# Optimization experiments

Hardware: AMD Instinct MI355X
Metric: run time of the kernel (lower is better)

The kernel has to match this reference:

```python
import jax, jax.numpy as jnp
import numpy as np

B, T_ENC, T_DEC, E = 16, 512, 128, 512
H = 1024


def setup_inputs() -> dict:
    key = jax.random.key(0)
    ks = jax.random.split(key, 16)
    def rn(k, shape, s=0.02):
        return jax.random.normal(k, shape, jnp.float32) * s
    z = lambda *s: jnp.zeros(s, jnp.float32)
    return {
        "inputs": jax.random.normal(ks[0], (B, T_ENC, E), jnp.float32),
        "padded_mels": jax.random.normal(ks[1], (B, 80, T_DEC), jnp.float32),
        "W_enc": rn(ks[2], (128, E)),
        "W_q": rn(ks[3], (128, H)),
        "W_loc_conv": rn(ks[4], (32, 1, 31)),
        "b_loc_conv": z(32),
        "W_loc_dense": rn(ks[5], (128, 32)),
        "b_loc_dense": z(128),
        "w_e": rn(ks[6], (1, 128)),
        "b_e": z(1),
        "W_p1": rn(ks[7], (256, 80)),
        "W_p2": rn(ks[8], (256, 256)),
        "W_ih1": rn(ks[9], (4 * H, 256 + E)),
        "W_hh1": rn(ks[10], (4 * H, H)),
        "b_ih1": z(4 * H),
        "b_hh1": z(4 * H),
        "W_ih2": rn(ks[11], (4 * H, H)),
        "W_hh2": rn(ks[12], (4 * H, H)),
        "b_ih2": z(4 * H),
        "b_hh2": z(4 * H),
        "W_proj": rn(ks[13], (80, H + E)),
        "b_proj": z(80),
        "W_stop": rn(ks[14], (1, H + E)),
        "b_stop": z(1),
    }


def _lstm_cell(x, h, c, W_ih, W_hh, b_ih, b_hh):
    g = W_ih @ x + b_ih + W_hh @ h + b_hh
    i, f, gg, o = jnp.split(g, 4)  # torch gate order: i, f, g, o
    c = jax.nn.sigmoid(f) * c + jax.nn.sigmoid(i) * jnp.tanh(gg)
    h = jax.nn.sigmoid(o) * jnp.tanh(c)
    return h, c


def _forward(inputs, padded_mels, W_enc, W_q, W_loc_conv, b_loc_conv,
             W_loc_dense, b_loc_dense, w_e, b_e, W_p1, W_p2,
             W_ih1, W_hh1, b_ih1, b_hh1, W_ih2, W_hh2, b_ih2, b_hh2,
             W_proj, b_proj, W_stop, b_stop):
    proc_enc = inputs @ W_enc.T  # (B, T_enc, 128)
    # prepend zero frame, use frames 0..T_dec-1 as teacher-forced inputs
    prev = jnp.concatenate([jnp.zeros((B, 80, 1), inputs.dtype), padded_mels], axis=-1)[:, :, :T_DEC]
    prev = jnp.transpose(prev, (2, 0, 1))  # (T_dec, B, 80)
    # F.dropout(p=0.5) in source defaults to training=True -> always applied; deterministic masks here
    mk = jax.random.key(42)
    m1 = jax.random.bernoulli(jax.random.fold_in(mk, 0), 0.5, (T_DEC, B, 256)).astype(inputs.dtype) * 2.0
    m2 = jax.random.bernoulli(jax.random.fold_in(mk, 1), 0.5, (T_DEC, B, 256)).astype(inputs.dtype) * 2.0

    def lstm2(x_seq):
        # faithful to source: (B,1,768) fed to batch_first=False nn.LSTM ->
        # sequence runs over the batch dim with batch=1 and zero init state each step
        zv = jnp.zeros((H,), x_seq.dtype)
        def cell(carry, x):
            h1, c1, h2, c2 = carry
            h1, c1 = _lstm_cell(x, h1, c1, W_ih1, W_hh1, b_ih1, b_hh1)
            h2, c2 = _lstm_cell(h1, h2, c2, W_ih2, W_hh2, b_ih2, b_hh2)
            return (h1, c1, h2, c2), h2
        _, hs = jax.lax.scan(cell, (zv, zv, zv, zv), x_seq)
        return hs  # (B, 1024)

    def step(carry, xs):
        cum, ctx = carry  # (B, T_enc), (B, E)
        x, d1, d2 = xs
        p = jax.nn.relu(x @ W_p1.T) * d1
        p = jax.nn.relu(p @ W_p2.T) * d2
        h = lstm2(jnp.concatenate([p, ctx], axis=-1))  # (B, 1024)
        q = h @ W_q.T  # (B, 128)
        loc = jax.lax.conv_general_dilated(
            cum[:, None, :], W_loc_conv, (1,), [(15, 15)],
            dimension_numbers=("NCH", "OIH", "NCH")) + b_loc_conv[None, :, None]  # (B, 32, T_enc)
        loc = jnp.transpose(loc, (0, 2, 1)) @ W_loc_dense.T + b_loc_dense  # (B, T_enc, 128)
        e = jnp.tanh(q[:, None, :] + loc + proc_enc) @ w_e[0] + b_e[0]  # (B, T_enc)
        aw = jax.nn.softmax(e, axis=1)
        new_ctx = jnp.einsum("bt,bte->be", aw, inputs)  # (B, E)
        do = jnp.concatenate([h, new_ctx], axis=-1)  # (B, 1536)
        frame = do @ W_proj.T + b_proj  # (B, 80)
        stop = do @ W_stop[0] + b_stop[0]  # (B,)
        return (cum + aw, new_ctx), (frame, stop)

    carry0 = (jnp.zeros((B, T_ENC), inputs.dtype), jnp.zeros((B, E), inputs.dtype))
    _, (mels, stops) = jax.lax.scan(step, carry0, (prev, m1, m2))
    return jnp.transpose(mels, (1, 0, 2)), jnp.transpose(stops, (1, 0))


def reference(inputs, padded_mels, W_enc, W_q, W_loc_conv, b_loc_conv,
              W_loc_dense, b_loc_dense, w_e, b_e, W_p1, W_p2,
              W_ih1, W_hh1, b_ih1, b_hh1, W_ih2, W_hh2, b_ih2, b_hh2,
              W_proj, b_proj, W_stop, b_stop):
    return _forward(inputs, padded_mels, W_enc, W_q, W_loc_conv, b_loc_conv,
                    W_loc_dense, b_loc_dense, w_e, b_e, W_p1, W_p2,
                    W_ih1, W_hh1, b_ih1, b_hh1, W_ih2, W_hh2, b_ih2, b_hh2,
                    W_proj, b_proj, W_stop, b_stop)
```

## Files before the change

kernel.cpp:

```cpp
#include <hip/hip_runtime.h>
#include <hip/hip_bf16.h>
#include <stdint.h>

#define TD 128
#define NB 16
#define TE 512
#define EE 512
#define HH 1024
#define NM 80
#define PP 256
#define NWG 256
#define NTH 512

#define AGENT __HIP_MEMORY_SCOPE_AGENT

__device__ inline float aloadf(const float* p) {
  return __hip_atomic_load(p, __ATOMIC_RELAXED, AGENT);
}
__device__ inline void astoref(float* p, float v) {
  __hip_atomic_store(p, v, __ATOMIC_RELAXED, AGENT);
}
__device__ inline double aloadd(const double* p) {
  return __hip_atomic_load(p, __ATOMIC_RELAXED, AGENT);
}
__device__ inline void astored(double* p, double v) {
  __hip_atomic_store(p, v, __ATOMIC_RELAXED, AGENT);
}
__device__ inline float2 aload2f(const float* p) {
  unsigned long long v =
      __hip_atomic_load((const unsigned long long*)p, __ATOMIC_RELAXED, AGENT);
  union { unsigned long long u; float2 f; } c; c.u = v; return c.f;
}
__device__ inline double dsig(double x) { return 1.0 / (1.0 + exp(-x)); }

__host__ __device__ inline void threefry2x32(uint32_t k0, uint32_t k1,
                                             uint32_t& x0, uint32_t& x1) {
  uint32_t ks0 = k0, ks1 = k1, ks2 = k0 ^ k1 ^ 0x1BD11BDAu;
  x0 += ks0; x1 += ks1;
#define RND(rot) { x0 += x1; x1 = (x1 << (rot)) | (x1 >> (32 - (rot))); x1 ^= x0; }
  RND(13) RND(15) RND(26) RND(6)
  x0 += ks1; x1 += ks2 + 1u;
  RND(17) RND(29) RND(16) RND(24)
  x0 += ks2; x1 += ks0 + 2u;
  RND(13) RND(15) RND(26) RND(6)
  x0 += ks0; x1 += ks1 + 3u;
  RND(17) RND(29) RND(16) RND(24)
  x0 += ks1; x1 += ks2 + 4u;
  RND(13) RND(15) RND(26) RND(6)
  x0 += ks2; x1 += ks0 + 5u;
#undef RND
}

__device__ inline double mask_val(uint32_t ka, uint32_t kb, uint32_t i) {
  uint32_t x0 = 0u, x1 = i;
  threefry2x32(ka, kb, x0, x1);
  uint32_t bits = x0 ^ x1;
  float u = __uint_as_float((bits >> 9) | 0x3f800000u) - 1.0f;
  return (u < 0.5f) ? 2.0 : 0.0;
}

__global__ void k_proc_enc(const float* __restrict__ inputs,
                           const float* __restrict__ W_enc,
                           float* __restrict__ procTf) {
  int blk = blockIdx.x;
  int b = blk >> 5;
  int t0 = (blk & 31) * 16;
  int d = threadIdx.x;
  __shared__ float in_l[16][EE];
  for (int idx = threadIdx.x; idx < 16 * EE; idx += blockDim.x) {
    int tt = idx >> 9, e = idx & 511;
    in_l[tt][e] = inputs[((size_t)(b * TE + t0 + tt)) * EE + e];
  }
  __syncthreads();
  double acc[16];
#pragma unroll
  for (int tt = 0; tt < 16; ++tt) acc[tt] = 0.0;
  const float* wr = W_enc + (size_t)d * EE;
  for (int e = 0; e < EE; ++e) {
    double w = (double)wr[e];
#pragma unroll
    for (int tt = 0; tt < 16; ++tt) acc[tt] += w * (double)in_l[tt][e];
  }
  for (int tt = 0; tt < 16; ++tt)
    procTf[((size_t)(b * 128 + d)) * TE + t0 + tt] = (float)acc[tt];
}

__global__ void k_p(const float* __restrict__ pm, const float* __restrict__ Wp1,
                    const float* __restrict__ Wp2,
                    uint32_t k1a, uint32_t k1b, uint32_t k2a, uint32_t k2b,
                    float* __restrict__ p_allf) {
  int sb = blockIdx.x;
  int s = sb >> 4, b = sb & 15;
  int tid = threadIdx.x;
  uint32_t mi = (uint32_t)(sb * PP + tid);
  double d1 = mask_val(k1a, k1b, mi);
  double d2 = mask_val(k2a, k2b, mi);
  __shared__ float x_l[NM];
  __shared__ double p1_l[PP];
  if (tid < NM) x_l[tid] = (s == 0) ? 0.f : pm[(b * NM + tid) * TD + (s - 1)];
  __syncthreads();
  double a = 0.0;
  const float* w1 = Wp1 + tid * NM;
  for (int m = 0; m < NM; ++m) a += (double)w1[m] * (double)x_l[m];
  a = fmax(a, 0.0) * d1;
  p1_l[tid] = a;
  __syncthreads();
  double c = 0.0;
  const float* w2 = Wp2 + tid * PP;
  for (int k = 0; k < PP; ++k) c += (double)w2[k] * p1_l[k];
  c = fmax(c, 0.0) * d2;
  p_allf[sb * PP + tid] = (float)c;
}

__global__ void k_init(double* __restrict__ cumg, float* __restrict__ ctxf,
                       float* __restrict__ h1f, float* __restrict__ h2f,
                       uint32_t* __restrict__ barmem) {
  int tid = threadIdx.x;
  for (int i = tid; i < NB * TE; i += 256) cumg[i] = 0.0;
  for (int i = tid; i < NB * EE; i += 256) ctxf[i] = 0.f;
  for (int i = tid; i < 2 * HH; i += 256) { h1f[i] = 0.f; h2f[i] = 0.f; }
  for (int i = tid; i < 1024; i += 256) barmem[i] = 0u;
}

struct SMEM {
  float wldT[4096];
  float wcl[992];
  double bld[128], we[128], blc[32];
  double b1l[16], b2l[16];
  double g1l[16][16];
  double gA[16], gBC[16];
  double c1l[4], c2l[4];
  double be0;
  union U {
    struct { float h1[1024], h2[1024]; } cell;
    struct { float h[1024]; } pq;
    struct { float ctxall[8192]; double x[768]; } g1p;
    struct { double cum[64], q[128], loc[32][33]; } att;
    struct { float aw[512]; double red[16][32]; } ctxp;
    struct { double red[16]; } soft;
    struct { float hb[1536]; double red[16]; } outp;
  } u;
};

__device__ inline void gridbar(uint32_t* barmem, uint32_t& lgen, int wg, int tid) {
  __syncthreads();
  lgen++;
  if (tid == 0) {
    int g = wg & 7;
    uint32_t a = __hip_atomic_fetch_add(&barmem[g * 32], 1u, __ATOMIC_RELAXED, AGENT);
    if (a == 31u) {
      uint32_t b = __hip_atomic_fetch_add(&barmem[256], 1u, __ATOMIC_RELAXED, AGENT);
      if (b == 7u) {
        for (int i = 0; i < 8; ++i)
          __hip_atomic_store(&barmem[i * 32], 0u, __ATOMIC_RELAXED, AGENT);
        __hip_atomic_store(&barmem[256], 0u, __ATOMIC_RELAXED, AGENT);
        asm volatile("s_waitcnt vmcnt(0)" ::: "memory");
        __hip_atomic_store(&barmem[288], lgen, __ATOMIC_RELAXED, AGENT);
      }
    }
    while (__hip_atomic_load(&barmem[288], __ATOMIC_RELAXED, AGENT) < lgen)
      __builtin_amdgcn_s_sleep(2);
  }
  __syncthreads();
}

__global__ __launch_bounds__(NTH)
__attribute__((amdgpu_waves_per_eu(2, 2)))
void k_persist(
    const float* __restrict__ inputs,
    const float* __restrict__ W_q,
    const float* __restrict__ W_lc, const float* __restrict__ b_lc,
    const float* __restrict__ W_ld, const float* __restrict__ b_ld,
    const float* __restrict__ w_e, const float* __restrict__ b_e,
    const float* __restrict__ W_ih1, const float* __restrict__ W_hh1,
    const float* __restrict__ b_ih1, const float* __restrict__ b_hh1,
    const float* __restrict__ W_ih2, const float* __restrict__ W_hh2,
    const float* __restrict__ b_ih2, const float* __restrict__ b_hh2,
    const float* __restrict__ W_proj, const float* __restrict__ b_proj,
    const float* __restrict__ W_stop, const float* __restrict__ b_stop,
    const float* __restrict__ p_allf, const float* __restrict__ procTf,
    float* h1f, float* h2f, float* h_allf, float* qf,
    float* ef, float* awf, double* cumg, float* ctxf,
    uint32_t* barmem, float* out) {
  __shared__ SMEM sm;
  const int wg = blockIdx.x, tid = threadIdx.x;
  const int q = tid >> 5, l = tid & 31;
  const int row = (q >> 2) * 1024 + wg * 4 + (q & 3);
  uint32_t lgen = 0;

  for (int i = tid; i < 4096; i += NTH) sm.wldT[(i & 31) * 128 + (i >> 5)] = W_ld[i];
  for (int i = tid; i < 992; i += NTH) sm.wcl[i] = W_lc[i];
  for (int i = tid; i < 128; i += NTH) { sm.bld[i] = (double)b_ld[i]; sm.we[i] = (double)w_e[i]; }
  if (tid < 32) sm.blc[tid] = (double)b_lc[tid];
  if (tid == 0) sm.be0 = (double)b_e[0];
  if (l == 0) {
    sm.b1l[q] = (double)b_ih1[row] + (double)b_hh1[row];
    sm.b2l[q] = (double)b_ih2[row] + (double)b_hh2[row];
  }

  float wA[32], wB[32], wC[32], wD[24];
#pragma unroll
  for (int k = 0; k < 32; ++k) {
    int c = l + 32 * k;
    wA[k] = W_hh1[(size_t)row * 1024 + c];
    wB[k] = W_ih2[(size_t)row * 1024 + c];
    wC[k] = W_hh2[(size_t)row * 1024 + c];
  }
#pragma unroll
  for (int k = 0; k < 24; ++k) wD[k] = W_ih1[(size_t)row * 768 + l + 32 * k];
#pragma unroll
  for (int k = 0; k < 32; ++k) {
    asm volatile("" : "+v"(wA[k]));
    asm volatile("" : "+v"(wB[k]));
    asm volatile("" : "+v"(wC[k]));
  }
#pragma unroll
  for (int k = 0; k < 24; ++k) asm volatile("" : "+v"(wD[k]));
  __syncthreads();

  {
    for (int i = tid; i < 8192; i += NTH) sm.u.g1p.ctxall[i] = aloadf(ctxf + i);
    __syncthreads();
    for (int b = 0; b < 16; ++b) {
      for (int i = tid; i < 768; i += NTH)
        sm.u.g1p.x[i] = (i < 256) ? (double)p_allf[((size_t)0 * 16 + b) * 256 + i]
                                  : (double)sm.u.g1p.ctxall[b * 512 + (i - 256)];
      __syncthreads();
      double a = 0.0;
#pragma unroll
      for (int k = 0; k < 24; ++k) a += (double)wD[k] * sm.u.g1p.x[l + 32 * k];
#pragma unroll
      for (int m = 1; m <= 16; m <<= 1) a += __shfl_xor(a, m);
      if (l == 0) sm.g1l[b][q] = a + sm.b1l[q];
      __syncthreads();
    }
  }
  gridbar(barmem, lgen, wg, tid);

  for (int s = 0; s < TD; ++s) {
    for (int r = 0; r <= 16; ++r) {
      if (r == 0 && tid < 4) { sm.c1l[tid] = 0.0; sm.c2l[tid] = 0.0; }
      {
        float2 v1 = aload2f(h1f + (((r & 1) ^ 1)) * 1024 + 2 * tid);
        sm.u.cell.h1[2 * tid] = v1.x; sm.u.cell.h1[2 * tid + 1] = v1.y;
        if (r > 0) {
          float2 v2 = aload2f(h2f + (r & 1) * 1024 + 2 * tid);
          sm.u.cell.h2[2 * tid] = v2.x; sm.u.cell.h2[2 * tid + 1] = v2.y;
        }
      }
      __syncthreads();

      double a0 = 0.0, a1 = 0.0, a2 = 0.0;
#pragma unroll
      for (int k = 0; k < 32; ++k) {
        double h1v = (double)sm.u.cell.h1[l + 32 * k];
        a0 += (double)wA[k] * h1v;
        a1 += (double)wB[k] * h1v;
        a2 += (double)wC[k] * (double)sm.u.cell.h2[l + 32 * k];
      }
#pragma unroll
      for (int m = 1; m <= 16; m <<= 1) {
        a0 += __shfl_xor(a0, m);
        a1 += __shfl_xor(a1, m);
        a2 += __shfl_xor(a2, m);
      }
      if (l == 0) { sm.gA[q] = a0; sm.gBC[q] = a1 + a2; }
      __syncthreads();

      if (r < 16 && tid < 4) {
        int jj = tid;
        double gi = sm.g1l[r][jj]      + sm.gA[jj];
        double gf = sm.g1l[r][4 + jj]  + sm.gA[4 + jj];
        double gg = sm.g1l[r][8 + jj]  + sm.gA[8 + jj];
        double go = sm.g1l[r][12 + jj] + sm.gA[12 + jj];
        double cn = dsig(gf) * sm.c1l[jj] + dsig(gi) * tanh(gg);
        double hn = dsig(go) * tanh(cn);
        sm.c1l[jj] = cn;
        astoref(h1f + (r & 1) * 1024 + wg * 4 + jj, (float)hn);
      }
      if (r > 0 && tid >= 8 && tid < 12) {
        int jj = tid - 8, b = r - 1;
        double gi = sm.gBC[jj]      + sm.b2l[jj];
        double gf = sm.gBC[4 + jj]  + sm.b2l[4 + jj];
        double gg = sm.gBC[8 + jj]  + sm.b2l[8 + jj];
        double go = sm.gBC[12 + jj] + sm.b2l[12 + jj];
        double cn = dsig(gf) * sm.c2l[jj] + dsig(gi) * tanh(gg);
        double hn = dsig(go) * tanh(cn);
        sm.c2l[jj] = cn;
        astoref(h2f + ((b & 1)) * 1024 + wg * 4 + jj, (float)hn);
        astoref(h_allf + (size_t)b * 1024 + wg * 4 + jj, (float)hn);
      }
      gridbar(barmem, lgen, wg, tid);
    }

    {
      int b = wg >> 4;
      float2 v = aload2f(h_allf + (size_t)b * 1024 + 2 * tid);
      sm.u.pq.h[2 * tid] = v.x; sm.u.pq.h[2 * tid + 1] = v.y;
      __syncthreads();
      int o = tid >> 6, lane = tid & 63;
      int d = (wg & 15) * 8 + o;
      double a = 0.0;
#pragma unroll
      for (int k = 0; k < 16; ++k) {
        int c = lane + 64 * k;
        a += (double)W_q[(size_t)d * 1024 + c] * (double)sm.u.pq.h[c];
      }
#pragma unroll
      for (int m = 1; m <= 32; m <<= 1) a += __shfl_xor(a, m);
      if (lane == 0) astoref(qf + b * 128 + d, (float)a);
    }
    gridbar(barmem, lgen, wg, tid);

    {
      int b = wg >> 4, t0 = (wg & 15) * 32;
      if (tid < 62) {
        int g = t0 - 15 + tid;
        sm.u.att.cum[tid] = (g >= 0 && g < TE) ? aloadd(cumg + b * TE + g) : 0.0;
      } else if (tid < 190) {
        sm.u.att.q[tid - 62] = (double)aloadf(qf + b * 128 + (tid - 62));
      }
      __syncthreads();
#pragma unroll
      for (int it = 0; it < 2; ++it) {
        int task = tid + it * NTH;
        int t = task >> 5, ch = task & 31;
        double v = sm.blc[ch];
#pragma unroll
        for (int k = 0; k < 31; ++k) v += (double)sm.wcl[ch * 31 + k] * sm.u.att.cum[t + k];
        sm.u.att.loc[t][ch] = v;
      }
      __syncthreads();
      int t = tid >> 4, part = tid & 15;
      double en = 0.0;
      for (int k = 0; k < 8; ++k) {
        int d = part + 16 * k;
        double sv = sm.u.att.q[d] + sm.bld[d] +
                    (double)procTf[((size_t)(b * 128 + d)) * TE + t0 + t];
#pragma unroll
        for (int c = 0; c < 32; ++c)
          sv += sm.u.att.loc[t][c] * (double)sm.wldT[c * 128 + d];
        en += tanh(sv) * sm.we[d];
      }
#pragma unroll
      for (int m = 1; m <= 8; m <<= 1) en += __shfl_xor(en, m);
      if (part == 0) astoref(ef + b * TE + t0 + t, (float)(en + sm.be0));
    }
    gridbar(barmem, lgen, wg, tid);

    if (wg < 16) {
      int b = wg;
      double e = (double)aloadf(ef + b * TE + tid);
      double mx = e;
#pragma unroll
      for (int m = 1; m <= 32; m <<= 1) mx = fmax(mx, __shfl_xor(mx, m));
      if ((tid & 63) == 0) sm.u.soft.red[tid >> 6] = mx;
      __syncthreads();
      if (tid == 0) {
        double mm = sm.u.soft.red[0];
        for (int i = 1; i < 8; ++i) mm = fmax(mm, sm.u.soft.red[i]);
        sm.u.soft.red[0] = mm;
      }
      __syncthreads();
      double p = exp(e - sm.u.soft.red[0]);
      __syncthreads();
      double ssum = p;
#pragma unroll
      for (int m = 1; m <= 32; m <<= 1) ssum += __shfl_xor(ssum, m);
      if ((tid & 63) == 0) sm.u.soft.red[tid >> 6] = ssum;
      __syncthreads();
      if (tid == 0) {
        double t_ = 0.0;
        for (int i = 0; i < 8; ++i) t_ += sm.u.soft.red[i];
        sm.u.soft.red[0] = 1.0 / t_;
      }
      __syncthreads();
      double a = p * sm.u.soft.red[0];
      astoref(awf + b * TE + tid, (float)a);
      astored(cumg + b * TE + tid, aloadd(cumg + b * TE + tid) + a);
    }
    gridbar(barmem, lgen, wg, tid);

    {
      int b = wg >> 4, e0 = (wg & 15) * 32;
      sm.u.ctxp.aw[tid] = aloadf(awf + b * TE + tid);
      __syncthreads();
      int e = e0 + (tid & 31), tp = tid >> 5;
      double a = 0.0;
      for (int t = tp * 32; t < tp * 32 + 32; ++t)
        a += (double)sm.u.ctxp.aw[t] * (double)inputs[((size_t)(b * TE + t)) * EE + e];
      sm.u.ctxp.red[tp][tid & 31] = a;
      __syncthreads();
      if (tid < 32) {
        double v = 0.0;
        for (int j = 0; j < 16; ++j) v += sm.u.ctxp.red[j][tid];
        astoref(ctxf + b * EE + e0 + tid, (float)v);
      }
    }
    gridbar(barmem, lgen, wg, tid);

    {
      int b = wg & 15, obase = wg >> 4;
      for (int i = tid; i < 1536; i += NTH)
        sm.u.outp.hb[i] = (i < 1024) ? aloadf(h_allf + (size_t)b * 1024 + i)
                                     : aloadf(ctxf + b * EE + (i - 1024));
      __syncthreads();
      for (int j = 0; j < 6; ++j) {
        int o = obase + 16 * j;
        if (o <= NM) {
          const float* wr = (o < NM) ? (W_proj + (size_t)o * 1536) : W_stop;
          double a = 0.0;
#pragma unroll
          for (int kk = 0; kk < 3; ++kk) {
            int k = tid + kk * NTH;
            a += (double)wr[k] * (double)sm.u.outp.hb[k];
          }
#pragma unroll
          for (int m = 1; m <= 32; m <<= 1) a += __shfl_xor(a, m);
          if ((tid & 63) == 0) sm.u.outp.red[tid >> 6] = a;
          __syncthreads();
          if (tid == 0) {
            double v = 0.0;
            for (int i = 0; i < 8; ++i) v += sm.u.outp.red[i];
            v += (o < NM) ? (double)b_proj[o] : (double)b_stop[0];
            if (o < NM) out[((size_t)b * TD + s) * NM + o] = (float)v;
            else        out[(size_t)NB * TD * NM + b * TD + s] = (float)v;
          }
          __syncthreads();
        }
      }
      __syncthreads();
      if (s < TD - 1) {
        const int ss = s + 1;
        for (int i = tid; i < 8192; i += NTH) sm.u.g1p.ctxall[i] = aloadf(ctxf + i);
        __syncthreads();
        for (int b2 = 0; b2 < 16; ++b2) {
          for (int i = tid; i < 768; i += NTH)
            sm.u.g1p.x[i] = (i < 256) ? (double)p_allf[((size_t)ss * 16 + b2) * 256 + i]
                                      : (double)sm.u.g1p.ctxall[b2 * 512 + (i - 256)];
          __syncthreads();
          double a = 0.0;
#pragma unroll
          for (int k = 0; k < 24; ++k) a += (double)wD[k] * sm.u.g1p.x[l + 32 * k];
#pragma unroll
          for (int m = 1; m <= 16; m <<= 1) a += __shfl_xor(a, m);
          if (l == 0) sm.g1l[b2][q] = a + sm.b1l[q];
          __syncthreads();
        }
        if (tid < 4) astoref(h1f + 1024 + wg * 4 + tid, 0.f);
        else if (tid < 8) astoref(h2f + 1024 + wg * 4 + (tid - 4), 0.f);
      }
    }
    gridbar(barmem, lgen, wg, tid);
  }
}

extern "C" void kernel_launch(void* const* d_in, const int* in_sizes, int n_in,
                              void* d_out, int out_size, void* d_ws, size_t ws_size,
                              hipStream_t stream) {
  const float* inputs = (const float*)d_in[0];
  const float* pmels  = (const float*)d_in[1];
  const float* W_enc  = (const float*)d_in[2];
  const float* W_q    = (const float*)d_in[3];
  const float* W_lc   = (const float*)d_in[4];
  const float* b_lc   = (const float*)d_in[5];
  const float* W_ld   = (const float*)d_in[6];
  const float* b_ld   = (const float*)d_in[7];
  const float* w_e    = (const float*)d_in[8];
  const float* b_e    = (const float*)d_in[9];
  const float* W_p1   = (const float*)d_in[10];
  const float* W_p2   = (const float*)d_in[11];
  const float* W_ih1  = (const float*)d_in[12];
  const float* W_hh1  = (const float*)d_in[13];
  const float* b_ih1  = (const float*)d_in[14];
  const float* b_hh1  = (const float*)d_in[15];
  const float* W_ih2  = (const float*)d_in[16];
  const float* W_hh2  = (const float*)d_in[17];
  const float* b_ih2  = (const float*)d_in[18];
  const float* b_hh2  = (const float*)d_in[19];
  const float* W_proj = (const float*)d_in[20];
  const float* b_proj = (const float*)d_in[21];
  const float* W_stop = (const float*)d_in[22];
  const float* b_stop = (const float*)d_in[23];
  float* out = (float*)d_out;

  float* ws     = (float*)d_ws;
  float* p_allf = ws;
  float* procTf = p_allf + 524288;
  float* h1f    = procTf + 1048576;
  float* h2f    = h1f + 2048;
  float* h_allf = h2f + 2048;
  float* qf     = h_allf + 16384;
  float* ef     = qf + 2048;
  float* awf    = ef + 8192;
  float* ctxf   = awf + 8192;
  double* cumg  = (double*)(ctxf + 8192);
  uint32_t* barmem = (uint32_t*)(cumg + 8192);

  uint32_t k1a = 0u, k1b = 0u, k2a = 0u, k2b = 1u;
  threefry2x32(0u, 42u, k1a, k1b);
  threefry2x32(0u, 42u, k2a, k2b);

  k_proc_enc<<<512, 128, 0, stream>>>(inputs, W_enc, procTf);
  k_p<<<TD * NB, 256, 0, stream>>>(pmels, W_p1, W_p2, k1a, k1b, k2a, k2b, p_allf);
  k_init<<<1, 256, 0, stream>>>(cumg, ctxf, h1f, h2f, barmem);

  k_persist<<<NWG, NTH, 0, stream>>>(
      inputs, W_q, W_lc, b_lc, W_ld, b_ld, w_e, b_e,
      W_ih1, W_hh1, b_ih1, b_hh1, W_ih2, W_hh2, b_ih2, b_hh2,
      W_proj, b_proj, W_stop, b_stop,
      p_allf, procTf, h1f, h2f, h_allf, qf, ef, awf, cumg, ctxf,
      barmem, out);

  (void)in_sizes; (void)n_in; (void)out_size; (void)ws_size;
}
```

Before: 33.25 ms.

## Replace hierarchical atomic grid barrier with flag-based barrier; drop per-batch staging syncs

Replaces the two-level atomic-counter grid barrier with a flag scheme. Each workgroup writes its generation to its own padded slot, workgroup 0 polls all of them, then releases everyone through a single broadcast flag. It also removes the per-batch shared-memory staging of the LSTM1 input vector, reading p_allf from global memory and ctx from shared memory directly. This cuts 32 __syncthreads per step down to one. The changes target barrier latency and intra-block sync overhead, at the cost of more global loads and a barrier that depends on a single master workgroup.

```diff
diff --git a/kernel.cpp b/kernel.cpp
--- a/kernel.cpp
+++ b/kernel.cpp
@@ -119,7 +119,7 @@
   for (int i = tid; i < NB * TE; i += 256) cumg[i] = 0.0;
   for (int i = tid; i < NB * EE; i += 256) ctxf[i] = 0.f;
   for (int i = tid; i < 2 * HH; i += 256) { h1f[i] = 0.f; h2f[i] = 0.f; }
-  for (int i = tid; i < 1024; i += 256) barmem[i] = 0u;
+  for (int i = tid; i < 8320; i += 256) barmem[i] = 0u;
 }
 
 struct SMEM {
@@ -134,7 +134,7 @@
   union U {
     struct { float h1[1024], h2[1024]; } cell;
     struct { float h[1024]; } pq;
-    struct { float ctxall[8192]; double x[768]; } g1p;
+    struct { float ctxall[8192]; } g1p;
     struct { double cum[64], q[128], loc[32][33]; } att;
     struct { float aw[512]; double red[16][32]; } ctxp;
     struct { double red[16]; } soft;
@@ -145,21 +145,23 @@
 __device__ inline void gridbar(uint32_t* barmem, uint32_t& lgen, int wg, int tid) {
   __syncthreads();
   lgen++;
-  if (tid == 0) {
-    int g = wg & 7;
-    uint32_t a = __hip_atomic_fetch_add(&barmem[g * 32], 1u, __ATOMIC_RELAXED, AGENT);
-    if (a == 31u) {
-      uint32_t b = __hip_atomic_fetch_add(&barmem[256], 1u, __ATOMIC_RELAXED, AGENT);
-      if (b == 7u) {
-        for (int i = 0; i < 8; ++i)
-          __hip_atomic_store(&barmem[i * 32], 0u, __ATOMIC_RELAXED, AGENT);
-        __hip_atomic_store(&barmem[256], 0u, __ATOMIC_RELAXED, AGENT);
-        asm volatile("s_waitcnt vmcnt(0)" ::: "memory");
-        __hip_atomic_store(&barmem[288], lgen, __ATOMIC_RELAXED, AGENT);
-      }
-    }
-    while (__hip_atomic_load(&barmem[288], __ATOMIC_RELAXED, AGENT) < lgen)
-      __builtin_amdgcn_s_sleep(2);
+  if (wg == 0) {
+    if (tid < 255) {
+      const uint32_t* fl = &barmem[(tid + 1) * 16];
+      while (__hip_atomic_load(fl, __ATOMIC_RELAXED, AGENT) < lgen)
+        __builtin_amdgcn_s_sleep(1);
+    }
+    __syncthreads();
+    if (tid == 0) {
+      asm volatile("s_waitcnt vmcnt(0)" ::: "memory");
+      __hip_atomic_store(&barmem[8192], lgen, __ATOMIC_RELAXED, AGENT);
+    }
+  } else {
+    if (tid == 0) {
+      __hip_atomic_store(&barmem[wg * 16], lgen, __ATOMIC_RELAXED, AGENT);
+      while (__hip_atomic_load(&barmem[8192], __ATOMIC_RELAXED, AGENT) < lgen)
+        __builtin_amdgcn_s_sleep(1);
+    }
   }
   __syncthreads();
 }
@@ -222,18 +224,18 @@
     for (int i = tid; i < 8192; i += NTH) sm.u.g1p.ctxall[i] = aloadf(ctxf + i);
     __syncthreads();
     for (int b = 0; b < 16; ++b) {
-      for (int i = tid; i < 768; i += NTH)
-        sm.u.g1p.x[i] = (i < 256) ? (double)p_allf[((size_t)0 * 16 + b) * 256 + i]
-                                  : (double)sm.u.g1p.ctxall[b * 512 + (i - 256)];
-      __syncthreads();
       double a = 0.0;
 #pragma unroll
-      for (int k = 0; k < 24; ++k) a += (double)wD[k] * sm.u.g1p.x[l + 32 * k];
+      for (int k = 0; k < 8; ++k)
+        a += (double)wD[k] * (double)p_allf[((size_t)0 * 16 + b) * 256 + l + 32 * k];
+#pragma unroll
+      for (int k = 8; k < 24; ++k)
+        a += (double)wD[k] * (double)sm.u.g1p.ctxall[b * 512 + l + 32 * k - 256];
 #pragma unroll
       for (int m = 1; m <= 16; m <<= 1) a += __shfl_xor(a, m);
       if (l == 0) sm.g1l[b][q] = a + sm.b1l[q];
-      __syncthreads();
-    }
+    }
+    __syncthreads();
   }
   gridbar(barmem, lgen, wg, tid);
 
@@ -435,18 +437,18 @@
         for (int i = tid; i < 8192; i += NTH) sm.u.g1p.ctxall[i] = aloadf(ctxf + i);
         __syncthreads();
         for (int b2 = 0; b2 < 16; ++b2) {
-          for (int i = tid; i < 768; i += NTH)
-            sm.u.g1p.x[i] = (i < 256) ? (double)p_allf[((size_t)ss * 16 + b2) * 256 + i]
-                                      : (double)sm.u.g1p.ctxall[b2 * 512 + (i - 256)];
-          __syncthreads();
           double a = 0.0;
 #pragma unroll
-          for (int k = 0; k < 24; ++k) a += (double)wD[k] * sm.u.g1p.x[l + 32 * k];
+          for (int k = 0; k < 8; ++k)
+            a += (double)wD[k] * (double)p_allf[((size_t)ss * 16 + b2) * 256 + l + 32 * k];
+#pragma unroll
+          for (int k = 8; k < 24; ++k)
+            a += (double)wD[k] * (double)sm.u.g1p.ctxall[b2 * 512 + l + 32 * k - 256];
 #pragma unroll
           for (int m = 1; m <= 16; m <<= 1) a += __shfl_xor(a, m);
           if (l == 0) sm.g1l[b2][q] = a + sm.b1l[q];
-          __syncthreads();
         }
+        __syncthreads();
         if (tid < 4) astoref(h1f + 1024 + wg * 4 + tid, 0.f);
         else if (tid < 8) astoref(h2f + 1024 + wg * 4 + (tid - 4), 0.f);
       }
```

After: 34.28 ms. 1.03x slower.
